# Kernel optimization log

Hardware: AMD Instinct MI355X
Metric: run time of the kernel (lower is better)

Reference implementation:

```python
import jax, jax.numpy as jnp
import numpy as np

INF = 1e20


def setup_inputs() -> dict:
    key = jax.random.key(0)
    k0, k1, k2, k3, k4 = jax.random.split(key, 5)
    B, T, C, D = 4, 8, 512, 256
    P, Ks = 4, 4
    return {
        "context": jax.random.normal(k0, (B, T, C, D), jnp.float32),
        "ctx_mask": jax.random.randint(k1, (B, C), 0, 2).astype(jnp.int32),
        "weight_tensor": jax.random.normal(k2, (P, D), jnp.float32),
        "mean_dis": jax.random.uniform(k3, (Ks, 1), jnp.float32),
        "precision_inv_dis": jax.random.uniform(k4, (Ks, 1), jnp.float32),
        "topk": 10,
        "max_position_distance": 160,
    }


def _forward(context, ctx_mask, weight_tensor, mean_dis, precision_inv_dis, topk, max_position_distance):
    B, T, C, D = context.shape
    Ks = mean_dis.shape[0]
    # attention[b,t,c,e] = mean_p sum_d ctx[b,t,c,d]*relu(W[p,d])*ctx[b,t,e,d]
    # (mean over perspectives commutes with the contraction over d)
    wbar = jnp.mean(jax.nn.relu(weight_tensor), axis=0)  # (D,)
    attention = jnp.einsum('btcd,bted->btce', context * wbar, context)  # (B,T,C,C)

    valid = ctx_mask > 0  # (B,C)
    pair_ok = valid[:, None, :, None] & valid[:, None, None, :]  # (B,1,C,C)
    attention = jnp.where(pair_ok, attention, -INF)

    # spatial Gaussian kernels over |i-j| distances (shared across batch/turn)
    idx = jnp.arange(C)
    pc = jnp.abs(idx[:, None] - idx[None, :]).astype(jnp.float32)
    pc = jnp.minimum(pc, float(max_position_distance)) / float(max_position_distance)  # (C,C)
    mu = mean_dis[:, 0][:, None, None]            # (Ks,1,1)
    prec = precision_inv_dis[:, 0][:, None, None]  # (Ks,1,1)
    spatial = jnp.exp(-0.5 * (pc[None] - mu) ** 2 * prec ** 2)  # (Ks,C,C)

    # kNN sparsification
    knn_val, knn_ind = jax.lax.top_k(attention, topk)  # (B,T,C,K)
    sem = jax.nn.softmax(knn_val, axis=-1)             # semantic weights (B,T,C,K)

    idx5 = jnp.broadcast_to(knn_ind[:, :, None, :, :], (B, T, Ks, C, topk))
    spatial_full = jnp.broadcast_to(spatial[None, None], (B, T, Ks, C, C))
    sp_chosen = jnp.take_along_axis(spatial_full, idx5, axis=-1)  # (B,T,Ks,C,K)
    sp_chosen = sp_chosen / jnp.sum(sp_chosen, axis=-1, keepdims=True)

    attn_chosen = sem[:, :, None, :, :] * sp_chosen  # (B,T,Ks,C,K)

    adj = jnp.zeros((B, T, Ks, C, C), dtype=attn_chosen.dtype)
    adj = adj.at[
        jnp.arange(B)[:, None, None, None, None],
        jnp.arange(T)[None, :, None, None, None],
        jnp.arange(Ks)[None, None, :, None, None],
        jnp.arange(C)[None, None, None, :, None],
        idx5,
    ].set(attn_chosen)
    return adj


def reference(context, ctx_mask, weight_tensor, mean_dis, precision_inv_dis, topk, max_position_distance):
    return _forward(context, ctx_mask, weight_tensor, mean_dis, precision_inv_dis, topk, max_position_distance)
```

## Files before the change

kernel.cpp:

```cpp
#include <hip/hip_runtime.h>
#include <math.h>

#define C_ 512
#define D_ 256
#define KS_ 4
#define TOPK_ 10
#define NEG 1e20f

typedef float v2f __attribute__((ext_vector_type(2)));
typedef float v4f __attribute__((ext_vector_type(4)));

__device__ __forceinline__ int csw2(int g) { return g ^ ((g >> 3) & 1); }

#define ASTR 36
#define BSTR2 260

#define PKFMA_LO(ACC, AP, BP) \
    asm("v_pk_fma_f32 %0, %1, %2, %0 op_sel:[0,0,0] op_sel_hi:[0,1,1]" \
        : "+v"(ACC) : "v"(AP), "v"(BP));
#define PKFMA_HI(ACC, AP, BP) \
    asm("v_pk_fma_f32 %0, %1, %2, %0 op_sel:[1,0,0] op_sel_hi:[1,1,1]" \
        : "+v"(ACC) : "v"(AP), "v"(BP));

extern "C" __global__ __launch_bounds__(256, 2)
void gemm_attn(const float* __restrict__ ctx,
               const float* __restrict__ W,
               float* __restrict__ ws)
{
    __shared__ __align__(16) float wbar_s[D_];
    __shared__ __align__(16) float a_s[16 * ASTR];
    __shared__ __align__(16) float b_s[16 * BSTR2];

    const int tid  = threadIdx.x;
    const int lane = tid & 63;
    const int wv   = tid >> 6;
    const int wr   = (wv >> 1) * 16;
    const int wc   = (wv & 1) * 128;
    const int rg   = lane >> 5;
    const int cg   = lane & 31;

    const int blk  = blockIdx.x;
    const int bt   = (blk & 7) * 4 + ((blk >> 3) & 3);
    const int tile = blk >> 5;
    const int c0   = (tile & 15) * 32;
    const int n0   = (tile >> 4) * 256;

    const float* ctx_bt = ctx + (size_t)bt * (C_ * D_);

    {
        float w0 = W[tid], w1 = W[D_ + tid], w2 = W[2 * D_ + tid], w3 = W[3 * D_ + tid];
        wbar_s[tid] = 0.25f * (fmaxf(w0, 0.f) + fmaxf(w1, 0.f) + fmaxf(w2, 0.f) + fmaxf(w3, 0.f));
    }

    const int bcol = tid >> 2;
    const int bq   = tid & 3;
    const float* bsrc = ctx_bt + (size_t)(n0 + bcol) * D_ + bq * 4;
    float* bdst = b_s + (4 * bq) * BSTR2 + bcol;
    const int ar_ = tid >> 2;
    const int aq  = tid & 3;
    const float* asrc = ctx_bt + (size_t)(c0 + ar_) * D_ + aq * 4;
    const int awbase = (4 * aq) * ASTR + ar_;
    const int abase = wr + rg * 8;
    const int bbase = wc + cg * 4;

    v2f acc2[8][2];
    #pragma unroll
    for (int j = 0; j < 8; ++j) { acc2[j][0] = (v2f){0.f, 0.f}; acc2[j][1] = (v2f){0.f, 0.f}; }

    v4f B0, B1, B2, B3, A0;
    B0 = *(const v4f*)(bsrc + (size_t)0 * 64 * D_);
    B1 = *(const v4f*)(bsrc + (size_t)1 * 64 * D_);
    B2 = *(const v4f*)(bsrc + (size_t)2 * 64 * D_);
    B3 = *(const v4f*)(bsrc + (size_t)3 * 64 * D_);
    if (tid < 128) A0 = *(const v4f*)asrc;

    for (int kt = 0; kt < 16; ++kt) {
        __syncthreads();
        #pragma unroll
        for (int j = 0; j < 4; ++j) {
            bdst[j * BSTR2 + 0 * 64] = B0[j];
            bdst[j * BSTR2 + 1 * 64] = B1[j];
            bdst[j * BSTR2 + 2 * 64] = B2[j];
            bdst[j * BSTR2 + 3 * 64] = B3[j];
        }
        if (tid < 128) {
            v4f wb = *(const v4f*)(wbar_s + kt * 16 + aq * 4);
            a_s[awbase + 0 * ASTR] = A0[0] * wb[0];
            a_s[awbase + 1 * ASTR] = A0[1] * wb[1];
            a_s[awbase + 2 * ASTR] = A0[2] * wb[2];
            a_s[awbase + 3 * ASTR] = A0[3] * wb[3];
        }
        __syncthreads();
        if (kt < 15) {
            const float* nb = bsrc + (kt + 1) * 16;
            B0 = *(const v4f*)(nb + (size_t)0 * 64 * D_);
            B1 = *(const v4f*)(nb + (size_t)1 * 64 * D_);
            B2 = *(const v4f*)(nb + (size_t)2 * 64 * D_);
            B3 = *(const v4f*)(nb + (size_t)3 * 64 * D_);
            if (tid < 128) A0 = *(const v4f*)(asrc + (kt + 1) * 16);
        }
        #pragma unroll
        for (int kk = 0; kk < 16; ++kk) {
            v4f av0 = *(const v4f*)(a_s + kk * ASTR + abase);
            v4f av1 = *(const v4f*)(a_s + kk * ASTR + abase + 4);
            v4f bv  = *(const v4f*)(b_s + kk * BSTR2 + bbase);
            v2f a01 = __builtin_shufflevector(av0, av0, 0, 1);
            v2f a23 = __builtin_shufflevector(av0, av0, 2, 3);
            v2f a45 = __builtin_shufflevector(av1, av1, 0, 1);
            v2f a67 = __builtin_shufflevector(av1, av1, 2, 3);
            v2f blo = __builtin_shufflevector(bv, bv, 0, 1);
            v2f bhi = __builtin_shufflevector(bv, bv, 2, 3);
            PKFMA_LO(acc2[0][0], a01, blo)  PKFMA_LO(acc2[0][1], a01, bhi)
            PKFMA_HI(acc2[1][0], a01, blo)  PKFMA_HI(acc2[1][1], a01, bhi)
            PKFMA_LO(acc2[2][0], a23, blo)  PKFMA_LO(acc2[2][1], a23, bhi)
            PKFMA_HI(acc2[3][0], a23, blo)  PKFMA_HI(acc2[3][1], a23, bhi)
            PKFMA_LO(acc2[4][0], a45, blo)  PKFMA_LO(acc2[4][1], a45, bhi)
            PKFMA_HI(acc2[5][0], a45, blo)  PKFMA_HI(acc2[5][1], a45, bhi)
            PKFMA_LO(acc2[6][0], a67, blo)  PKFMA_LO(acc2[6][1], a67, bhi)
            PKFMA_HI(acc2[7][0], a67, blo)  PKFMA_HI(acc2[7][1], a67, bhi)
        }
    }

    #pragma unroll
    for (int j = 0; j < 8; ++j) {
        v4f o = __builtin_shufflevector(acc2[j][0], acc2[j][1], 0, 1, 2, 3);
        *(v4f*)(ws + ((size_t)bt * C_ + c0 + wr + rg * 8 + j) * C_ + n0 + bbase) = o;
    }
}

extern "C" __global__ __launch_bounds__(256, 2)
void epilogue_k(const float* __restrict__ ws,
                const int* __restrict__ cmask,
                const float* __restrict__ mu_g,
                const float* __restrict__ pr_g,
                float* __restrict__ out)
{
    const int tid  = threadIdx.x;
    const int lane = tid & 63;
    const int wv   = tid >> 6;

    const int blk = blockIdx.x;
    const int bt  = blk >> 7;
    const int rq  = blk & 127;
    const int b   = bt >> 3;

    {
        const float4 z = make_float4(0.f, 0.f, 0.f, 0.f);
        #pragma unroll
        for (int ks = 0; ks < KS_; ++ks) {
            float* ob = out + ((size_t)(bt * KS_ + ks) * C_ + rq * 4) * C_;
            *(float4*)(ob + (size_t)tid * 4)         = z;
            *(float4*)(ob + (size_t)(tid + 256) * 4) = z;
        }
    }

    const int c  = rq * 4 + wv;
    const int vr = cmask[b * C_ + c];

    float row[8];
    {
        const float* wrow = ws + ((size_t)bt * C_ + c) * C_ + lane * 8;
        float4 r0 = *(const float4*)wrow;
        float4 r1 = *(const float4*)(wrow + 4);
        row[0] = r0.x; row[1] = r0.y; row[2] = r0.z; row[3] = r0.w;
        row[4] = r1.x; row[5] = r1.y; row[6] = r1.z; row[7] = r1.w;
        int4 m0 = *(const int4*)(cmask + b * C_ + lane * 8);
        int4 m1 = *(const int4*)(cmask + b * C_ + lane * 8 + 4);
        int em[8] = {m0.x, m0.y, m0.z, m0.w, m1.x, m1.y, m1.z, m1.w};
        #pragma unroll
        for (int i = 0; i < 8; ++i) {
            bool ok = (vr > 0) && (em[i] > 0);
            row[i] = ok ? row[i] : -NEG;
        }
    }

    float tv[TOPK_];
    int   te[TOPK_];
    unsigned int taken = 0;
    #pragma unroll
    for (int j = 0; j < TOPK_; ++j) {
        float lv = -3.3e38f;
        int   li = 0;
        #pragma unroll
        for (int i = 0; i < 8; ++i) {
            bool better = (!((taken >> i) & 1u)) && (row[i] > lv);
            lv = better ? row[i] : lv;
            li = better ? i : li;
        }
        int le = lane * 8 + li;
        #pragma unroll
        for (int off = 1; off < 64; off <<= 1) {
            float ov = __shfl_xor(lv, off);
            int   oe = __shfl_xor(le, off);
            bool take = (ov > lv) || (ov == lv && oe < le);
            lv = take ? ov : lv;
            le = take ? oe : le;
        }
        tv[j] = lv;
        te[j] = le;
        if ((le >> 3) == lane) taken |= 1u << (le & 7);
    }
    const float mx = tv[0];
    float ssum = 0.f;
    #pragma unroll
    for (int j = 0; j < TOPK_; ++j) ssum += expf(tv[j] - mx);

    float oval = 0.f;
    size_t ooff = 0;
    {
        const int ksq = (lane < 40) ? (lane / 10) : 3;
        const int myj = (lane < 40) ? (lane - (lane / 10) * 10) : 0;
        const float mu = mu_g[ksq];
        const float pr = pr_g[ksq];
        float sps = 0.f, spj = 0.f, tvj = 0.f;
        int ej = 0;
        #pragma unroll
        for (int j = 0; j < TOPK_; ++j) {
            float d = fabsf((float)(te[j] - c));
            d = fminf(d, 160.f) * (1.0f / 160.0f);
            float x  = d - mu;
            float sp = expf(-0.5f * x * x * pr * pr);
            sps += sp;
            if (j == myj) { spj = sp; tvj = tv[j]; ej = te[j]; }
        }
        oval = (expf(tvj - mx) / ssum) * (spj / sps);
        ooff = ((size_t)(bt * KS_ + ksq) * C_ + c) * C_ + ej;
    }

    __syncthreads();
    if (lane < 40) out[ooff] = oval;
}

#define BSTR 516
extern "C" __global__ __launch_bounds__(256, 2)
void graph_learner(const float* __restrict__ ctx,
                   const int* __restrict__ cmask,
                   const float* __restrict__ W,
                   const float* __restrict__ mu_g,
                   const float* __restrict__ pr_g,
                   float* __restrict__ out)
{
    __shared__ __align__(16) float wbar_s[D_];
    __shared__ __align__(16) float a_s[16 * ASTR];
    __shared__ __align__(16) float b_s[16 * BSTR];
    __shared__ __align__(8)  float res_s[2560];
    __shared__ unsigned int vmask_s[16];

    const int tid  = threadIdx.x;
    const int lane = tid & 63;
    const int wv   = tid >> 6;
    const int w8   = wv * 8;

    const int blk = blockIdx.x;
    const int bt  = (blk & 7) * 4 + ((blk >> 3) & 3);
    const int c0  = (blk >> 5) * 32;
    const int b   = bt >> 3;

    const float* ctx_bt = ctx + (size_t)bt * (C_ * D_);
    const int*   mask_b = cmask + b * C_;

    {
        float w0 = W[tid], w1 = W[D_ + tid], w2 = W[2 * D_ + tid], w3 = W[3 * D_ + tid];
        wbar_s[tid] = 0.25f * (fmaxf(w0, 0.f) + fmaxf(w1, 0.f) + fmaxf(w2, 0.f) + fmaxf(w3, 0.f));
    }
    if (tid < 16) {
        unsigned int m = 0;
        for (int i = 0; i < 32; ++i)
            m |= (mask_b[tid * 32 + i] > 0 ? 1u : 0u) << i;
        vmask_s[tid] = m;
    }

    const int brow = tid >> 2;
    const int bq   = tid & 3;
    const float* bsrc = ctx_bt + (size_t)brow * D_ + bq * 4;
    const int bwbase = (4 * bq) * BSTR + 4 * csw2(brow >> 2) + (brow & 3);
    const int ar_ = tid >> 2;
    const int aq  = tid & 3;
    const float* asrc = ctx_bt + (size_t)(c0 + ar_) * D_ + aq * 4;
    const int awbase = (4 * aq) * ASTR + ar_;
    const int bc0 = 4 * csw2(2 * lane);
    const int bc1 = 4 * csw2(2 * lane + 1);

    v2f acc2[8][4];
    #pragma unroll
    for (int j = 0; j < 8; ++j)
        #pragma unroll
        for (int t = 0; t < 4; ++t) acc2[j][t] = (v2f){0.f, 0.f};

    for (int kt = 0; kt < 16; ++kt) {
        __syncthreads();
        #pragma unroll
        for (int i = 0; i < 8; ++i) {
            float4 v = *(const float4*)(bsrc + (size_t)i * 64 * D_ + kt * 16);
            b_s[bwbase + 0 * BSTR + i * 64] = v.x;
            b_s[bwbase + 1 * BSTR + i * 64] = v.y;
            b_s[bwbase + 2 * BSTR + i * 64] = v.z;
            b_s[bwbase + 3 * BSTR + i * 64] = v.w;
        }
        if (tid < 128) {
            float4 v  = *(const float4*)(asrc + kt * 16);
            float4 wb = *(const float4*)(wbar_s + kt * 16 + aq * 4);
            a_s[awbase + 0 * ASTR] = v.x * wb.x;
            a_s[awbase + 1 * ASTR] = v.y * wb.y;
            a_s[awbase + 2 * ASTR] = v.z * wb.z;
            a_s[awbase + 3 * ASTR] = v.w * wb.w;
        }
        __syncthreads();
        #pragma unroll
        for (int kk = 0; kk < 16; ++kk) {
            float4 av0 = *(const float4*)(a_s + kk * ASTR + w8);
            float4 av1 = *(const float4*)(a_s + kk * ASTR + w8 + 4);
            float4 bv0 = *(const float4*)(b_s + kk * BSTR + bc0);
            float4 bv1 = *(const float4*)(b_s + kk * BSTR + bc1);
            v2f b20 = (v2f){bv0.x, bv0.y};
            v2f b21 = (v2f){bv0.z, bv0.w};
            v2f b22 = (v2f){bv1.x, bv1.y};
            v2f b23 = (v2f){bv1.z, bv1.w};
            float ar8[8] = {av0.x, av0.y, av0.z, av0.w, av1.x, av1.y, av1.z, av1.w};
            #pragma unroll
            for (int j = 0; j < 8; ++j) {
                v2f a2 = (v2f){ar8[j], ar8[j]};
                asm("v_pk_fma_f32 %0, %1, %2, %0" : "+v"(acc2[j][0]) : "v"(a2), "v"(b20));
                asm("v_pk_fma_f32 %0, %1, %2, %0" : "+v"(acc2[j][1]) : "v"(a2), "v"(b21));
                asm("v_pk_fma_f32 %0, %1, %2, %0" : "+v"(acc2[j][2]) : "v"(a2), "v"(b22));
                asm("v_pk_fma_f32 %0, %1, %2, %0" : "+v"(acc2[j][3]) : "v"(a2), "v"(b23));
            }
        }
    }

    {
        const float4 z = make_float4(0.f, 0.f, 0.f, 0.f);
        #pragma unroll
        for (int ks = 0; ks < KS_; ++ks) {
            float* ob = out + ((size_t)(bt * KS_ + ks) * C_ + c0) * C_;
            #pragma unroll
            for (int i = 0; i < 16; ++i)
                *(float4*)(ob + (size_t)(tid + i * 256) * 4) = z;
        }
    }

    const unsigned int em8 = (vmask_s[lane >> 2] >> ((lane & 3) * 8)) & 0xffu;
    const float mu0 = mu_g[0], mu1 = mu_g[1], mu2 = mu_g[2], mu3 = mu_g[3];
    const float pr0 = pr_g[0], pr1 = pr_g[1], pr2 = pr_g[2], pr3 = pr_g[3];

    #pragma unroll
    for (int jr = 0; jr < 8; ++jr) {
        const int c  = c0 + w8 + jr;
        const int vr = mask_b[c];
        float row[8];
        #pragma unroll
        for (int t = 0; t < 4; ++t) { row[2 * t] = acc2[jr][t].x; row[2 * t + 1] = acc2[jr][t].y; }
        #pragma unroll
        for (int i = 0; i < 8; ++i) {
            bool ok = (vr > 0) && ((em8 >> i) & 1u);
            row[i] = ok ? row[i] : -NEG;
        }
        float tv[TOPK_];
        int   te[TOPK_];
        unsigned int taken = 0;
        #pragma unroll
        for (int j = 0; j < TOPK_; ++j) {
            float lv = -3.3e38f;
            int   li = 0;
            #pragma unroll
            for (int i = 0; i < 8; ++i) {
                bool better = (!((taken >> i) & 1u)) && (row[i] > lv);
                lv = better ? row[i] : lv;
                li = better ? i : li;
            }
            int le = lane * 8 + li;
            #pragma unroll
            for (int off = 1; off < 64; off <<= 1) {
                float ov = __shfl_xor(lv, off);
                int   oe = __shfl_xor(le, off);
                bool take = (ov > lv) || (ov == lv && oe < le);
                lv = take ? ov : lv;
                le = take ? oe : le;
            }
            tv[j] = lv;
            te[j] = le;
            if ((le >> 3) == lane) taken |= 1u << (le & 7);
        }
        const float mx = tv[0];
        float ssum = 0.f;
        #pragma unroll
        for (int j = 0; j < TOPK_; ++j) ssum += expf(tv[j] - mx);

        if (lane < 40) {
            const int ksq = lane / 10;
            const int myj = lane - ksq * 10;
            const float mu = (ksq == 0) ? mu0 : (ksq == 1) ? mu1 : (ksq == 2) ? mu2 : mu3;
            const float pr = (ksq == 0) ? pr0 : (ksq == 1) ? pr1 : (ksq == 2) ? pr2 : pr3;
            float sps = 0.f, spj = 0.f, tvj = 0.f;
            int ej = 0;
            #pragma unroll
            for (int j = 0; j < TOPK_; ++j) {
                float d = fabsf((float)(te[j] - c));
                d = fminf(d, 160.f) * (1.0f / 160.0f);
                float x  = d - mu;
                float sp = expf(-0.5f * x * x * pr * pr);
                sps += sp;
                if (j == myj) { spj = sp; tvj = tv[j]; ej = te[j]; }
            }
            float val = (expf(tvj - mx) / ssum) * (spj / sps);
            int   off = ((bt * KS_ + ksq) * C_ + c) * C_ + ej;
            int   slot = (((wv * 8 + jr) * 40) + lane) * 2;
            res_s[slot]     = val;
            res_s[slot + 1] = __int_as_float(off);
        }
    }

    __syncthreads();
    #pragma unroll
    for (int i = 0; i < 5; ++i) {
        int p = tid * 5 + i;
        float v   = res_s[2 * p];
        int   off = __float_as_int(res_s[2 * p + 1]);
        out[off] = v;
    }
}

extern "C" void kernel_launch(void* const* d_in, const int* in_sizes, int n_in,
                              void* d_out, int out_size, void* d_ws, size_t ws_size,
                              hipStream_t stream) {
    (void)in_sizes; (void)n_in; (void)out_size;
    const float* ctx   = (const float*)d_in[0];
    const int*   cmask = (const int*)d_in[1];
    const float* W     = (const float*)d_in[2];
    const float* mu    = (const float*)d_in[3];
    const float* pr    = (const float*)d_in[4];
    const size_t WS_NEEDED = (size_t)32 * C_ * C_ * sizeof(float);
    if (ws_size >= WS_NEEDED) {
        float* ws = (float*)d_ws;
        gemm_attn<<<dim3(1024), dim3(256), 0, stream>>>(ctx, W, ws);
        epilogue_k<<<dim3(4096), dim3(256), 0, stream>>>(ws, cmask, mu, pr, (float*)d_out);
    } else {
        graph_learner<<<dim3(512), dim3(256), 0, stream>>>(ctx, cmask, W, mu, pr, (float*)d_out);
    }
}
```

Baseline: 96.66 us.

## Double-buffer LDS tiles in GEMM to drop one barrier per k-step

The attention GEMM kernel now keeps two LDS buffers for the A and B tiles. Each k-step computes from the current buffer and writes the prefetched next tile into the other buffer partway through the FMA loop, so only one barrier per iteration is needed instead of two. This targets barrier stalls and lets LDS stores overlap with compute, at the cost of doubled LDS use (about 37KB per block), which may limit occupancy.

Measured after the change: 97.49 us. About the same (+0.9%).

```diff
diff --git a/kernel.cpp b/kernel.cpp
--- a/kernel.cpp
+++ b/kernel.cpp
@@ -14,6 +14,8 @@
 
 #define ASTR 36
 #define BSTR2 260
+#define ABUF2 (16 * ASTR)
+#define BBUF2 (16 * BSTR2)
 
 #define PKFMA_LO(ACC, AP, BP) \
     asm("v_pk_fma_f32 %0, %1, %2, %0 op_sel:[0,0,0] op_sel_hi:[0,1,1]" \
@@ -28,8 +30,8 @@
                float* __restrict__ ws)
 {
     __shared__ __align__(16) float wbar_s[D_];
-    __shared__ __align__(16) float a_s[16 * ASTR];
-    __shared__ __align__(16) float b_s[16 * BSTR2];
+    __shared__ __align__(16) float a_s[2 * ABUF2];
+    __shared__ __align__(16) float b_s[2 * BBUF2];
 
     const int tid  = threadIdx.x;
     const int lane = tid & 63;
@@ -55,43 +57,74 @@
     const int bcol = tid >> 2;
     const int bq   = tid & 3;
     const float* bsrc = ctx_bt + (size_t)(n0 + bcol) * D_ + bq * 4;
-    float* bdst = b_s + (4 * bq) * BSTR2 + bcol;
+    const int bwoff = (4 * bq) * BSTR2 + bcol;
     const int ar_ = tid >> 2;
     const int aq  = tid & 3;
     const float* asrc = ctx_bt + (size_t)(c0 + ar_) * D_ + aq * 4;
-    const int awbase = (4 * aq) * ASTR + ar_;
+    const int awoff = (4 * aq) * ASTR + ar_;
     const int abase = wr + rg * 8;
     const int bbase = wc + cg * 4;
 
+    __syncthreads();
+
+    {
+        v4f B0 = *(const v4f*)(bsrc + (size_t)0 * 64 * D_);
+        v4f B1 = *(const v4f*)(bsrc + (size_t)1 * 64 * D_);
+        v4f B2 = *(const v4f*)(bsrc + (size_t)2 * 64 * D_);
+        v4f B3 = *(const v4f*)(bsrc + (size_t)3 * 64 * D_);
+        #pragma unroll
+        for (int j = 0; j < 4; ++j) {
+            b_s[bwoff + j * BSTR2 + 0 * 64] = B0[j];
+            b_s[bwoff + j * BSTR2 + 1 * 64] = B1[j];
+            b_s[bwoff + j * BSTR2 + 2 * 64] = B2[j];
+            b_s[bwoff + j * BSTR2 + 3 * 64] = B3[j];
+        }
+        if (tid < 128) {
+            v4f A0 = *(const v4f*)asrc;
+            v4f wb = *(const v4f*)(wbar_s + aq * 4);
+            a_s[awoff + 0 * ASTR] = A0[0] * wb[0];
+            a_s[awoff + 1 * ASTR] = A0[1] * wb[1];
+            a_s[awoff + 2 * ASTR] = A0[2] * wb[2];
+            a_s[awoff + 3 * ASTR] = A0[3] * wb[3];
+        }
+    }
+    __syncthreads();
+
     v2f acc2[8][2];
     #pragma unroll
     for (int j = 0; j < 8; ++j) { acc2[j][0] = (v2f){0.f, 0.f}; acc2[j][1] = (v2f){0.f, 0.f}; }
 
-    v4f B0, B1, B2, B3, A0;
-    B0 = *(const v4f*)(bsrc + (size_t)0 * 64 * D_);
-    B1 = *(const v4f*)(bsrc + (size_t)1 * 64 * D_);
-    B2 = *(const v4f*)(bsrc + (size_t)2 * 64 * D_);
-    B3 = *(const v4f*)(bsrc + (size_t)3 * 64 * D_);
-    if (tid < 128) A0 = *(const v4f*)asrc;
+    #define FMA_RANGE(K0, K1)                                                 \
+        _Pragma("unroll")                                                     \
+        for (int kk = (K0); kk < (K1); ++kk) {                                \
+            v4f av0 = *(const v4f*)(acur + kk * ASTR + abase);                \
+            v4f av1 = *(const v4f*)(acur + kk * ASTR + abase + 4);            \
+            v4f bv  = *(const v4f*)(bcur + kk * BSTR2 + bbase);               \
+            v2f a01 = __builtin_shufflevector(av0, av0, 0, 1);                \
+            v2f a23 = __builtin_shufflevector(av0, av0, 2, 3);                \
+            v2f a45 = __builtin_shufflevector(av1, av1, 0, 1);                \
+            v2f a67 = __builtin_shufflevector(av1, av1, 2, 3);                \
+            v2f blo = __builtin_shufflevector(bv, bv, 0, 1);                  \
+            v2f bhi = __builtin_shufflevector(bv, bv, 2, 3);                  \
+            PKFMA_LO(acc2[0][0], a01, blo)  PKFMA_LO(acc2[0][1], a01, bhi)    \
+            PKFMA_HI(acc2[1][0], a01, blo)  PKFMA_HI(acc2[1][1], a01, bhi)    \
+            PKFMA_LO(acc2[2][0], a23, blo)  PKFMA_LO(acc2[2][1], a23, bhi)    \
+            PKFMA_HI(acc2[3][0], a23, blo)  PKFMA_HI(acc2[3][1], a23, bhi)    \
+            PKFMA_LO(acc2[4][0], a45, blo)  PKFMA_LO(acc2[4][1], a45, bhi)    \
+            PKFMA_HI(acc2[5][0], a45, blo)  PKFMA_HI(acc2[5][1], a45, bhi)    \
+            PKFMA_LO(acc2[6][0], a67, blo)  PKFMA_LO(acc2[6][1], a67, bhi)    \
+            PKFMA_HI(acc2[7][0], a67, blo)  PKFMA_HI(acc2[7][1], a67, bhi)    \
+        }
 
     for (int kt = 0; kt < 16; ++kt) {
-        __syncthreads();
-        #pragma unroll
-        for (int j = 0; j < 4; ++j) {
-            bdst[j * BSTR2 + 0 * 64] = B0[j];
-            bdst[j * BSTR2 + 1 * 64] = B1[j];
-            bdst[j * BSTR2 + 2 * 64] = B2[j];
-            bdst[j * BSTR2 + 3 * 64] = B3[j];
-        }
-        if (tid < 128) {
-            v4f wb = *(const v4f*)(wbar_s + kt * 16 + aq * 4);
-            a_s[awbase + 0 * ASTR] = A0[0] * wb[0];
-            a_s[awbase + 1 * ASTR] = A0[1] * wb[1];
-            a_s[awbase + 2 * ASTR] = A0[2] * wb[2];
-            a_s[awbase + 3 * ASTR] = A0[3] * wb[3];
-        }
-        __syncthreads();
-        if (kt < 15) {
+        const float* acur = a_s + (kt & 1) * ABUF2;
+        const float* bcur = b_s + (kt & 1) * BBUF2;
+        float* anx = a_s + ((kt & 1) ^ 1) * ABUF2;
+        float* bnx = b_s + ((kt & 1) ^ 1) * BBUF2;
+        const bool pf = (kt < 15);
+
+        v4f B0, B1, B2, B3, A0;
+        if (pf) {
             const float* nb = bsrc + (kt + 1) * 16;
             B0 = *(const v4f*)(nb + (size_t)0 * 64 * D_);
             B1 = *(const v4f*)(nb + (size_t)1 * 64 * D_);
@@ -99,27 +132,27 @@
             B3 = *(const v4f*)(nb + (size_t)3 * 64 * D_);
             if (tid < 128) A0 = *(const v4f*)(asrc + (kt + 1) * 16);
         }
-        #pragma unroll
-        for (int kk = 0; kk < 16; ++kk) {
-            v4f av0 = *(const v4f*)(a_s + kk * ASTR + abase);
-            v4f av1 = *(const v4f*)(a_s + kk * ASTR + abase + 4);
-            v4f bv  = *(const v4f*)(b_s + kk * BSTR2 + bbase);
-            v2f a01 = __builtin_shufflevector(av0, av0, 0, 1);
-            v2f a23 = __builtin_shufflevector(av0, av0, 2, 3);
-            v2f a45 = __builtin_shufflevector(av1, av1, 0, 1);
-            v2f a67 = __builtin_shufflevector(av1, av1, 2, 3);
-            v2f blo = __builtin_shufflevector(bv, bv, 0, 1);
-            v2f bhi = __builtin_shufflevector(bv, bv, 2, 3);
-            PKFMA_LO(acc2[0][0], a01, blo)  PKFMA_LO(acc2[0][1], a01, bhi)
-            PKFMA_HI(acc2[1][0], a01, blo)  PKFMA_HI(acc2[1][1], a01, bhi)
-            PKFMA_LO(acc2[2][0], a23, blo)  PKFMA_LO(acc2[2][1], a23, bhi)
-            PKFMA_HI(acc2[3][0], a23, blo)  PKFMA_HI(acc2[3][1], a23, bhi)
-            PKFMA_LO(acc2[4][0], a45, blo)  PKFMA_LO(acc2[4][1], a45, bhi)
-            PKFMA_HI(acc2[5][0], a45, blo)  PKFMA_HI(acc2[5][1], a45, bhi)
-            PKFMA_LO(acc2[6][0], a67, blo)  PKFMA_LO(acc2[6][1], a67, bhi)
-            PKFMA_HI(acc2[7][0], a67, blo)  PKFMA_HI(acc2[7][1], a67, bhi)
-        }
-    }
+        FMA_RANGE(0, 10)
+        if (pf) {
+            #pragma unroll
+            for (int j = 0; j < 4; ++j) {
+                bnx[bwoff + j * BSTR2 + 0 * 64] = B0[j];
+                bnx[bwoff + j * BSTR2 + 1 * 64] = B1[j];
+                bnx[bwoff + j * BSTR2 + 2 * 64] = B2[j];
+                bnx[bwoff + j * BSTR2 + 3 * 64] = B3[j];
+            }
+            if (tid < 128) {
+                v4f wb = *(const v4f*)(wbar_s + (kt + 1) * 16 + aq * 4);
+                anx[awoff + 0 * ASTR] = A0[0] * wb[0];
+                anx[awoff + 1 * ASTR] = A0[1] * wb[1];
+                anx[awoff + 2 * ASTR] = A0[2] * wb[2];
+                anx[awoff + 3 * ASTR] = A0[3] * wb[3];
+            }
+        }
+        FMA_RANGE(10, 16)
+        __syncthreads();
+    }
+    #undef FMA_RANGE
 
     #pragma unroll
     for (int j = 0; j < 8; ++j) {
```
